# Kernel optimization log

Measured on AMD Instinct MI355X. Metric: run time of the kernel, lower is better.

The kernel has to match this reference:

```python
import jax, jax.numpy as jnp
import numpy as np
from jax import lax

B, C, W, H = 32, 64, 32, 32
HEADS, RED = 4, 16
D = C // HEADS


def setup_inputs() -> dict:
    key = jax.random.key(0)
    ks = jax.random.split(key, 16)
    s = 0.05
    return {
        "x": jax.random.normal(ks[0], (B, C, W, H), jnp.float32),
        "Wq": jax.random.normal(ks[1], (C, C), jnp.float32) * s,
        "bq": jnp.zeros((C,), jnp.float32),
        "Wk": jax.random.normal(ks[2], (C, C), jnp.float32) * s,
        "bk": jnp.zeros((C,), jnp.float32),
        "Wv": jax.random.normal(ks[3], (C, C), jnp.float32) * s,
        "bv": jnp.zeros((C,), jnp.float32),
        "rel_h": jax.random.normal(ks[4], (1, HEADS, D, 1, H), jnp.float32),
        "rel_w": jax.random.normal(ks[5], (1, HEADS, D, W, 1), jnp.float32),
        "ln_g": jnp.ones((C, W, H), jnp.float32),
        "ln_b": jnp.zeros((C, W, H), jnp.float32),
        "ca_w1": jax.random.normal(ks[6], (C // RED, C), jnp.float32) * s,
        "ca_b1": jnp.zeros((C // RED,), jnp.float32),
        "ca_w2": jax.random.normal(ks[7], (C, C // RED), jnp.float32) * s,
        "ca_b2": jnp.zeros((C,), jnp.float32),
        "sa_w": jax.random.normal(ks[8], (1, 2, 7, 7), jnp.float32) * s,
        "sa_b": jnp.zeros((1,), jnp.float32),
    }


def reference(x, Wq, bq, Wk, bk, Wv, bv, rel_h, rel_w, ln_g, ln_b,
              ca_w1, ca_b1, ca_w2, ca_b2, sa_w, sa_b):
    b, c, w, h = x.shape
    n = w * h
    d = c // HEADS

    def conv1x1(t, wt, bt):
        return jnp.einsum('bchw,oc->bohw', t, wt) + bt[None, :, None, None]

    # ---- MHSA branch ----
    q = conv1x1(x, Wq, bq).reshape(b, HEADS, d, n)
    k = conv1x1(x, Wk, bk).reshape(b, HEADS, d, n)
    v = conv1x1(x, Wv, bv).reshape(b, HEADS, d, n)
    cc = jnp.einsum('bhdi,bhdj->bhij', q, k)                  # content-content
    pos = (rel_h + rel_w).reshape(1, HEADS, d, n)              # [1,H,d,N]
    cp = jnp.einsum('zhdi,bhdj->bhij', pos, q)                 # content-position
    att = jax.nn.softmax(cc + cp, axis=-1)                     # [b,H,N,N]
    out = jnp.einsum('bhdj,bhij->bhdi', v, att).reshape(b, c, w, h)
    # LayerNorm over (C,W,H)
    mu = jnp.mean(out, axis=(1, 2, 3), keepdims=True)
    var = jnp.var(out, axis=(1, 2, 3), keepdims=True)
    ln = (out - mu) * lax.rsqrt(var + 1e-5) * ln_g[None] + ln_b[None]
    mhsa = ln + x

    # ---- CBAM branch ----
    avg = jnp.mean(x, axis=(2, 3))                             # [b,c]
    mx = jnp.max(x, axis=(2, 3))

    def mlp(f):
        hid = jax.nn.relu(jnp.einsum('bc,oc->bo', f, ca_w1) + ca_b1)
        return jnp.einsum('bc,oc->bo', hid, ca_w2) + ca_b2

    ch_att = jax.nn.sigmoid(mlp(avg) + mlp(mx))[:, :, None, None]
    xc = ch_att * x
    feat = jnp.stack([jnp.mean(xc, axis=1), jnp.max(xc, axis=1)], axis=1)  # [b,2,w,h]
    sp = lax.conv_general_dilated(feat, sa_w, (1, 1), 'SAME',
                                  dimension_numbers=('NCHW', 'OIHW', 'NCHW'))
    sp = sp + sa_b[None, :, None, None]
    cbam = jax.nn.sigmoid(sp) * xc

    return mhsa + cbam + x
```

## Files before the change

### kernel.cpp

```cpp
#include <hip/hip_runtime.h>

#define BB 32
#define CC 64
#define WW 32
#define HHT 32
#define NH 4
#define DHD 16
#define NN 1024
#define LOG2E 1.4426950408889634f

typedef __attribute__((ext_vector_type(8))) short bf16x8;
typedef __attribute__((ext_vector_type(4))) float f32x4;

__device__ __forceinline__ float wave_sum(float v) {
#pragma unroll
  for (int off = 32; off > 0; off >>= 1) v += __shfl_down(v, off, 64);
  return v;
}
__device__ __forceinline__ float wave_max(float v) {
#pragma unroll
  for (int off = 32; off > 0; off >>= 1) v = fmaxf(v, __shfl_down(v, off, 64));
  return v;
}
__device__ __forceinline__ unsigned bf16pair(float lo, float hi) {
  unsigned a = __float_as_uint(lo), b = __float_as_uint(hi);
  a += 0x7FFFu + ((a >> 16) & 1u);
  b += 0x7FFFu + ((b >> 16) & 1u);
  return (a >> 16) | (b & 0xFFFF0000u);
}
__device__ __forceinline__ unsigned bf16pair_trunc(float lo, float hi) {
  return __builtin_amdgcn_perm(__float_as_uint(hi), __float_as_uint(lo), 0x07060302u);
}
__device__ __forceinline__ short bf16s(float f) {
  unsigned a = __float_as_uint(f);
  a += 0x7FFFu + ((a >> 16) & 1u);
  return (short)(a >> 16);
}

__global__ __launch_bounds__(256) void qkv_kernel(
    const float* __restrict__ x,
    const float* __restrict__ Wq, const float* __restrict__ bq,
    const float* __restrict__ Wk, const float* __restrict__ bk,
    const float* __restrict__ Wv, const float* __restrict__ bv,
    short* __restrict__ KQ, short* __restrict__ Vb, float* __restrict__ lnzero)
{
  __shared__ __align__(16) short Ws[192 * 72];
  const int tid = threadIdx.x;
  const int b = blockIdx.y, nt = blockIdx.x;

  if (tid < 192) {
    const int m = tid >> 4, dd = tid & 15;
    const int mat = m >> 2, h = m & 3;
    const float* src = (mat == 0 ? Wk : (mat == 1 ? Wq : Wv)) + (h * 16 + dd) * CC;
    const float scale = (mat == 0) ? LOG2E : 1.f;
    short* dst = Ws + tid * 72;
#pragma unroll
    for (int c8 = 0; c8 < 8; ++c8) {
      const float4 f0 = *reinterpret_cast<const float4*>(src + c8 * 8);
      const float4 f1 = *reinterpret_cast<const float4*>(src + c8 * 8 + 4);
      uint4 u;
      u.x = bf16pair(f0.x*scale, f0.y*scale); u.y = bf16pair(f0.z*scale, f0.w*scale);
      u.z = bf16pair(f1.x*scale, f1.y*scale); u.w = bf16pair(f1.z*scale, f1.w*scale);
      *reinterpret_cast<uint4*>(dst + c8 * 8) = u;
    }
  }
  if (blockIdx.x == 0 && blockIdx.y == 0 && tid < 64) lnzero[tid] = 0.f;
  __syncthreads();

  const int wid = tid >> 6, lane = tid & 63, Q = lane >> 4, il = lane & 15;
  const int n = nt * 64 + wid * 16 + il;
  const float* xb = x + (size_t)b * CC * NN;

  union { bf16x8 s; unsigned u[4]; } bfr[2];
#pragma unroll
  for (int half = 0; half < 2; ++half) {
#pragma unroll
    for (int p = 0; p < 4; ++p) {
      const int c0 = 32 * half + 8 * Q + 2 * p;
      const float f0 = xb[(size_t)c0 * NN + n];
      const float f1 = xb[(size_t)(c0 + 1) * NN + n];
      bfr[half].u[p] = bf16pair(f0, f1);
    }
  }

  const f32x4 zero4 = {0.f, 0.f, 0.f, 0.f};
  f32x4 acc[12];
#pragma unroll
  for (int m = 0; m < 12; ++m) {
    const short* wr = Ws + (m * 16 + il) * 72;
    const bf16x8 a0 = *reinterpret_cast<const bf16x8*>(wr + 8 * Q);
    const bf16x8 a1 = *reinterpret_cast<const bf16x8*>(wr + 32 + 8 * Q);
    acc[m] = __builtin_amdgcn_mfma_f32_16x16x32_bf16(a0, bfr[0].s, zero4, 0, 0, 0);
    acc[m] = __builtin_amdgcn_mfma_f32_16x16x32_bf16(a1, bfr[1].s, acc[m], 0, 0, 0);
  }

#pragma unroll
  for (int m = 0; m < 12; ++m) {
    const int mat = m >> 2, h = m & 3;
    const float bsc = (mat == 0) ? LOG2E : 1.f;
    const float4 bias = *reinterpret_cast<const float4*>(
        (mat == 0 ? bk : (mat == 1 ? bq : bv)) + h * 16 + 4 * Q);
    const float v0 = acc[m][0] + bias.x*bsc, v1 = acc[m][1] + bias.y*bsc;
    const float v2 = acc[m][2] + bias.z*bsc, v3 = acc[m][3] + bias.w*bsc;
    if (mat < 2) {
      uint2 pk;
      pk.x = bf16pair(v0, v1); pk.y = bf16pair(v2, v3);
      *reinterpret_cast<uint2*>(KQ + ((size_t)(b * NH + h) * NN + n) * 32 +
                                (mat == 0 ? 0 : 16) + 4 * Q) = pk;
    } else {
      short* vb = Vb + ((size_t)(b * NH + h) * 16 + 4 * Q) * NN + n;
      vb[0]            = bf16s(v0);
      vb[(size_t)NN]   = bf16s(v1);
      vb[2*(size_t)NN] = bf16s(v2);
      vb[3*(size_t)NN] = bf16s(v3);
    }
  }
}

__global__ __launch_bounds__(256, 2) void flash_kernel(
    const short* __restrict__ KQ, const short* __restrict__ Vb,
    const float* __restrict__ rel_h, const float* __restrict__ rel_w,
    float* __restrict__ attnout, float* __restrict__ lnsum, float* __restrict__ lnsum2)
{
  const int tid = threadIdx.x;
  const int wid = tid >> 6, lane = tid & 63;
  const int Q = lane >> 4, il = lane & 15;
  const int bh = blockIdx.x;
  const int h = bh & 3, b = bh >> 2;
  const int ibase = blockIdx.y * 256 + wid * 64;

  bf16x8 bfrag[4];
#pragma unroll
  for (int g2 = 0; g2 < 4; ++g2) {
    const int i = ibase + g2*16 + il;
    if (Q < 2) {
      bfrag[g2] = *reinterpret_cast<const bf16x8*>(KQ + ((size_t)bh*NN + i)*32 + 16 + 8*Q);
    } else {
      const int wrow = i >> 5, hcol = i & 31;
      union { bf16x8 s; unsigned u[4]; } t;
#pragma unroll
      for (int p = 0; p < 4; ++p) {
        const int d0 = 8*(Q-2) + 2*p;
        const float f0 = LOG2E*(rel_h[(h*DHD + d0)*HHT + hcol] + rel_w[(h*DHD + d0)*WW + wrow]);
        const float f1 = LOG2E*(rel_h[(h*DHD + d0+1)*HHT + hcol] + rel_w[(h*DHD + d0+1)*WW + wrow]);
        t.u[p] = bf16pair(f0, f1);
      }
      bfrag[g2] = t.s;
    }
  }

  const short* KQb = KQ + (size_t)bh*NN*32;
  const short* Vbb = Vb + ((size_t)bh*16 + il)*NN;
  const f32x4 zero4 = {0.f, 0.f, 0.f, 0.f};
  f32x4 accA[4] = {zero4, zero4, zero4, zero4};
  f32x4 accB[4] = {zero4, zero4, zero4, zero4};
  float lpA[4] = {0.f, 0.f, 0.f, 0.f};
  float lpB[4] = {0.f, 0.f, 0.f, 0.f};

  bf16x8 agA[4], agB[4]; uint2 vloA[2], vhiA[2], vloB[2], vhiB[2];
#pragma unroll
  for (int g = 0; g < 4; ++g) {
    agA[g] = *reinterpret_cast<const bf16x8*>(KQb + (size_t)(      16*g + il)*32 + 8*Q);
    agB[g] = *reinterpret_cast<const bf16x8*>(KQb + (size_t)(512 + 16*g + il)*32 + 8*Q);
  }
#pragma unroll
  for (int hh = 0; hh < 2; ++hh) {
    const short* vpA = Vbb + 32*hh + 4*Q;
    const short* vpB = Vbb + 512 + 32*hh + 4*Q;
    vloA[hh] = *reinterpret_cast<const uint2*>(vpA);
    vhiA[hh] = *reinterpret_cast<const uint2*>(vpA + 16);
    vloB[hh] = *reinterpret_cast<const uint2*>(vpB);
    vhiB[hh] = *reinterpret_cast<const uint2*>(vpB + 16);
  }

  for (int jt = 0; jt < 512; jt += 64) {
    const int jn = (jt + 64) & 511;
    bf16x8 agAn[4], agBn[4]; uint2 vloAn[2], vhiAn[2], vloBn[2], vhiBn[2];
#pragma unroll
    for (int g = 0; g < 4; ++g) {
      agAn[g] = *reinterpret_cast<const bf16x8*>(KQb + (size_t)(      jn + 16*g + il)*32 + 8*Q);
      agBn[g] = *reinterpret_cast<const bf16x8*>(KQb + (size_t)(512 + jn + 16*g + il)*32 + 8*Q);
    }
#pragma unroll
    for (int hh = 0; hh < 2; ++hh) {
      const short* vpA = Vbb + jn + 32*hh + 4*Q;
      const short* vpB = Vbb + 512 + jn + 32*hh + 4*Q;
      vloAn[hh] = *reinterpret_cast<const uint2*>(vpA);
      vhiAn[hh] = *reinterpret_cast<const uint2*>(vpA + 16);
      vloBn[hh] = *reinterpret_cast<const uint2*>(vpB);
      vhiBn[hh] = *reinterpret_cast<const uint2*>(vpB + 16);
    }

    union { bf16x8 s; unsigned u[4]; } bvA0, bvA1, bvB0, bvB1;
    bvA0.u[0] = vloA[0].x; bvA0.u[1] = vloA[0].y; bvA0.u[2] = vhiA[0].x; bvA0.u[3] = vhiA[0].y;
    bvA1.u[0] = vloA[1].x; bvA1.u[1] = vloA[1].y; bvA1.u[2] = vhiA[1].x; bvA1.u[3] = vhiA[1].y;
    bvB0.u[0] = vloB[0].x; bvB0.u[1] = vloB[0].y; bvB0.u[2] = vhiB[0].x; bvB0.u[3] = vhiB[0].y;
    bvB1.u[0] = vloB[1].x; bvB1.u[1] = vloB[1].y; bvB1.u[2] = vhiB[1].x; bvB1.u[3] = vhiB[1].y;

#pragma unroll
    for (int g2 = 0; g2 < 4; ++g2) {
      {
        float p[4][4];
        unsigned pk[4][2];
#pragma unroll
        for (int g = 0; g < 4; ++g) {
          const f32x4 s = __builtin_amdgcn_mfma_f32_16x16x32_bf16(agA[g], bfrag[g2], zero4, 0, 0, 0);
#pragma unroll
          for (int r = 0; r < 4; ++r) p[g][r] = __builtin_amdgcn_exp2f(s[r]);
          lpA[g2] += (p[g][0] + p[g][1]) + (p[g][2] + p[g][3]);
          pk[g][0] = bf16pair_trunc(p[g][0], p[g][1]);
          pk[g][1] = bf16pair_trunc(p[g][2], p[g][3]);
        }
#pragma unroll
        for (int hh = 0; hh < 2; ++hh) {
          union { bf16x8 s; unsigned u[4]; } ap;
          ap.u[0] = pk[2*hh][0];   ap.u[1] = pk[2*hh][1];
          ap.u[2] = pk[2*hh+1][0]; ap.u[3] = pk[2*hh+1][1];
          accA[g2] = __builtin_amdgcn_mfma_f32_16x16x32_bf16(ap.s, hh ? bvA1.s : bvA0.s, accA[g2], 0, 0, 0);
        }
      }
      {
        float p[4][4];
        unsigned pk[4][2];
#pragma unroll
        for (int g = 0; g < 4; ++g) {
          const f32x4 s = __builtin_amdgcn_mfma_f32_16x16x32_bf16(agB[g], bfrag[g2], zero4, 0, 0, 0);
#pragma unroll
          for (int r = 0; r < 4; ++r) p[g][r] = __builtin_amdgcn_exp2f(s[r]);
          lpB[g2] += (p[g][0] + p[g][1]) + (p[g][2] + p[g][3]);
          pk[g][0] = bf16pair_trunc(p[g][0], p[g][1]);
          pk[g][1] = bf16pair_trunc(p[g][2], p[g][3]);
        }
#pragma unroll
        for (int hh = 0; hh < 2; ++hh) {
          union { bf16x8 s; unsigned u[4]; } ap;
          ap.u[0] = pk[2*hh][0];   ap.u[1] = pk[2*hh][1];
          ap.u[2] = pk[2*hh+1][0]; ap.u[3] = pk[2*hh+1][1];
          accB[g2] = __builtin_amdgcn_mfma_f32_16x16x32_bf16(ap.s, hh ? bvB1.s : bvB0.s, accB[g2], 0, 0, 0);
        }
      }
    }
#pragma unroll
    for (int g = 0; g < 4; ++g) { agA[g] = agAn[g]; agB[g] = agBn[g]; }
#pragma unroll
    for (int hh = 0; hh < 2; ++hh) {
      vloA[hh] = vloAn[hh]; vhiA[hh] = vhiAn[hh];
      vloB[hh] = vloBn[hh]; vhiB[hh] = vhiBn[hh];
    }
  }

  float s1 = 0.f, s2 = 0.f;
#pragma unroll
  for (int g2 = 0; g2 < 4; ++g2) {
    float l = lpA[g2] + lpB[g2];
    l += __shfl_xor(l, 16, 64);
    l += __shfl_xor(l, 32, 64);
#pragma unroll
    for (int r = 0; r < 4; ++r) {
      const float li = __shfl(l, 4*Q + r, 64);
      const float v = (accA[g2][r] + accB[g2][r]) / li;
      const int ig = ibase + g2*16 + 4*Q + r;
      attnout[((size_t)b*CC + h*DHD + il)*NN + ig] = v;
      s1 += v; s2 += v*v;
    }
  }
  s1 = wave_sum(s1); s2 = wave_sum(s2);
  __shared__ float r1[4], r2[4];
  if (lane == 0) { r1[wid] = s1; r2[wid] = s2; }
  __syncthreads();
  if (tid == 0) {
    atomicAdd(&lnsum[b],  r1[0]+r1[1]+r1[2]+r1[3]);
    atomicAdd(&lnsum2[b], r2[0]+r2[1]+r2[2]+r2[3]);
  }
}

__global__ __launch_bounds__(256) void cbamstats_kernel(
    const float* __restrict__ x, float* __restrict__ avg, float* __restrict__ mx)
{
  const int bc = blockIdx.x, tid = threadIdx.x;
  const float* p = x + (size_t)bc*NN;
  float s = 0.f, m = -3.0e38f;
  for (int u = tid; u < NN; u += 256) { const float v = p[u]; s += v; m = fmaxf(m, v); }
  s = wave_sum(s); m = wave_max(m);
  __shared__ float rs[4], rm[4];
  const int wid = tid >> 6, lane = tid & 63;
  if (lane == 0) { rs[wid] = s; rm[wid] = m; }
  __syncthreads();
  if (tid == 0) {
    avg[bc] = (rs[0]+rs[1]+rs[2]+rs[3]) * (1.f/NN);
    mx[bc]  = fmaxf(fmaxf(rm[0], rm[1]), fmaxf(rm[2], rm[3]));
  }
}

__global__ __launch_bounds__(256) void mlpfeat_kernel(
    const float* __restrict__ x, const float* __restrict__ avg, const float* __restrict__ mxv,
    const float* __restrict__ w1, const float* __restrict__ b1,
    const float* __restrict__ w2, const float* __restrict__ b2,
    float* __restrict__ chv, float* __restrict__ feat)
{
  const int b = blockIdx.y, qq = blockIdx.x, tid = threadIdx.x;
  __shared__ float sa[CC], sm[CC], sch[CC];
  __shared__ float ps[4][64], pm[4][64];
  if (tid < CC) { sa[tid] = avg[b*CC + tid]; sm[tid] = mxv[b*CC + tid]; }
  __syncthreads();
  if (tid < CC) {
    float s = 2.f * b2[tid];
#pragma unroll
    for (int o = 0; o < 4; ++o) {
      float ha = b1[o], hm = b1[o];
#pragma unroll
      for (int k = 0; k < CC; ++k) { ha += w1[o*CC + k]*sa[k]; hm += w1[o*CC + k]*sm[k]; }
      s += w2[tid*4 + o] * (fmaxf(ha, 0.f) + fmaxf(hm, 0.f));
    }
    const float c = 1.f/(1.f + __expf(-s));
    sch[tid] = c;
    if (qq == 0) chv[b*CC + tid] = c;
  }
  __syncthreads();
  const int nl = tid & 63, cg = tid >> 6;
  const int n = qq*64 + nl;
  float s = 0.f, m = -3.0e38f;
#pragma unroll
  for (int c = cg*16; c < cg*16 + 16; ++c) {
    const float v = sch[c] * x[((size_t)b*CC + c)*NN + n];
    s += v; m = fmaxf(m, v);
  }
  ps[cg][nl] = s; pm[cg][nl] = m;
  __syncthreads();
  if (cg == 0) {
    const float S = ps[0][nl]+ps[1][nl]+ps[2][nl]+ps[3][nl];
    const float M = fmaxf(fmaxf(pm[0][nl], pm[1][nl]), fmaxf(pm[2][nl], pm[3][nl]));
    feat[(size_t)b*2*NN + n]      = S * (1.f/CC);
    feat[(size_t)b*2*NN + NN + n] = M;
  }
}

__global__ __launch_bounds__(256) void final_kernel(
    const float* __restrict__ x, const float* __restrict__ attn,
    const float* __restrict__ ln_g, const float* __restrict__ ln_b,
    const float* __restrict__ feat, const float* __restrict__ ch,
    const float* __restrict__ lnsum, const float* __restrict__ lnsum2,
    const float* __restrict__ sa_w, const float* __restrict__ sa_b,
    float* __restrict__ out)
{
  const int b = blockIdx.y;
  const int c0 = blockIdx.z * 8;
  const int n = blockIdx.x*256 + threadIdx.x;
  const int w = n >> 5, hh = n & 31;
  __shared__ float sch[CC];
  __shared__ float swt[98];
  if (threadIdx.x < CC) sch[threadIdx.x] = ch[b*CC + threadIdx.x];
  if (threadIdx.x < 98) swt[threadIdx.x] = sa_w[threadIdx.x];
  __syncthreads();

  float s = sa_b[0];
#pragma unroll
  for (int ci = 0; ci < 2; ++ci)
#pragma unroll
    for (int kh = 0; kh < 7; ++kh) {
      const int wy = w + kh - 3;
      if (wy < 0 || wy >= WW) continue;
#pragma unroll
      for (int kw = 0; kw < 7; ++kw) {
        const int hx = hh + kw - 3;
        if (hx < 0 || hx >= HHT) continue;
        s += feat[((size_t)(b*2) + ci)*NN + wy*HHT + hx] * swt[ci*49 + kh*7 + kw];
      }
    }
  const float sg = 1.f/(1.f + __expf(-s));
  const float inv = 1.f/(CC*NN);
  const float m = lnsum[b]*inv;
  const float var = lnsum2[b]*inv - m*m;
  const float r = rsqrtf(var + 1e-5f);
#pragma unroll
  for (int c = c0; c < c0 + 8; ++c) {
    const size_t idx = ((size_t)b*CC + c)*NN + n;
    const float xa = x[idx];
    const float ln = (attn[idx] - m) * r * ln_g[c*NN + n] + ln_b[c*NN + n];
    out[idx] = ln + 2.f*xa + sg * sch[c] * xa;
  }
}

extern "C" void kernel_launch(void* const* d_in, const int* in_sizes, int n_in,
                              void* d_out, int out_size, void* d_ws, size_t ws_size,
                              hipStream_t stream)
{
  const float* x     = (const float*)d_in[0];
  const float* Wq    = (const float*)d_in[1];
  const float* bq    = (const float*)d_in[2];
  const float* Wk    = (const float*)d_in[3];
  const float* bk    = (const float*)d_in[4];
  const float* Wv    = (const float*)d_in[5];
  const float* bv    = (const float*)d_in[6];
  const float* rel_h = (const float*)d_in[7];
  const float* rel_w = (const float*)d_in[8];
  const float* ln_g  = (const float*)d_in[9];
  const float* ln_b  = (const float*)d_in[10];
  const float* cw1   = (const float*)d_in[11];
  const float* cb1   = (const float*)d_in[12];
  const float* cw2   = (const float*)d_in[13];
  const float* cb2   = (const float*)d_in[14];
  const float* saw   = (const float*)d_in[15];
  const float* sab   = (const float*)d_in[16];
  float* out = (float*)d_out;

  short* KQ = (short*)d_ws;
  short* Vb = KQ + (size_t)128*1024*32;
  float* fs = (float*)(Vb + (size_t)128*16*1024);
  float* lnsum  = fs;
  float* lnsum2 = fs + 32;
  float* avg    = fs + 64;
  float* mxv    = avg + 2048;
  float* chv    = mxv + 2048;
  float* feat   = chv + 2048;
  float* attn   = out;

  qkv_kernel<<<dim3(16, BB), 256, 0, stream>>>(x, Wq, bq, Wk, bk, Wv, bv, KQ, Vb, lnsum);
  flash_kernel<<<dim3(BB*NH, 4), 256, 0, stream>>>(KQ, Vb, rel_h, rel_w, attn, lnsum, lnsum2);
  cbamstats_kernel<<<BB*CC, 256, 0, stream>>>(x, avg, mxv);
  mlpfeat_kernel<<<dim3(16, BB), 256, 0, stream>>>(x, avg, mxv, cw1, cb1, cw2, cb2, chv, feat);
  final_kernel<<<dim3(4, BB, 8), 256, 0, stream>>>(x, attn, ln_g, ln_b, feat, chv, lnsum, lnsum2, saw, sab, out);
}
```

Before: 175.2 us.

## Split key range across two wave groups and merge partial attention through LDS

The flash kernel now launches 512 threads per block. The two halves of the block each process half of the key/value range for the same 256 queries, which doubles the number of waves in flight to hide exp and MFMA latency. Partial outputs and row sums are combined in shared memory, then written with coalesced float4 stores using a reciprocal instead of a divide. The cost is extra LDS traffic, a block barrier, and higher register pressure from the tighter launch bounds.

```diff
diff --git a/kernel.cpp b/kernel.cpp
--- a/kernel.cpp
+++ b/kernel.cpp
@@ -11,6 +11,8 @@
 
 typedef __attribute__((ext_vector_type(8))) short bf16x8;
 typedef __attribute__((ext_vector_type(4))) float f32x4;
+
+union vfrag_t { bf16x8 s; uint2 d[2]; unsigned u[4]; };
 
 __device__ __forceinline__ float wave_sum(float v) {
 #pragma unroll
@@ -117,17 +119,24 @@
   }
 }
 
-__global__ __launch_bounds__(256, 2) void flash_kernel(
+#define OSTRIDE 260
+__global__ __launch_bounds__(512, 4) void flash_kernel(
     const short* __restrict__ KQ, const short* __restrict__ Vb,
     const float* __restrict__ rel_h, const float* __restrict__ rel_w,
     float* __restrict__ attnout, float* __restrict__ lnsum, float* __restrict__ lnsum2)
 {
+  __shared__ __align__(16) float Olds[2*16*OSTRIDE];
+  __shared__ float lpl[2*256];
+  __shared__ float r1[8], r2[8];
   const int tid = threadIdx.x;
   const int wid = tid >> 6, lane = tid & 63;
   const int Q = lane >> 4, il = lane & 15;
+  const int jh = wid >> 2, iquad = wid & 3;
   const int bh = blockIdx.x;
   const int h = bh & 3, b = bh >> 2;
-  const int ibase = blockIdx.y * 256 + wid * 64;
+  const int iblk = blockIdx.y * 256;
+  const int ibase = iblk + iquad * 64;
+  const int jbase = jh * 512;
 
   bf16x8 bfrag[4];
 #pragma unroll
@@ -137,7 +146,7 @@
       bfrag[g2] = *reinterpret_cast<const bf16x8*>(KQ + ((size_t)bh*NN + i)*32 + 16 + 8*Q);
     } else {
       const int wrow = i >> 5, hcol = i & 31;
-      union { bf16x8 s; unsigned u[4]; } t;
+      vfrag_t t;
 #pragma unroll
       for (int p = 0; p < 4; ++p) {
         const int d0 = 8*(Q-2) + 2*p;
@@ -149,53 +158,49 @@
     }
   }
 
-  const short* KQb = KQ + (size_t)bh*NN*32;
-  const short* Vbb = Vb + ((size_t)bh*16 + il)*NN;
+  const short* KQb = KQ + (size_t)bh*NN*32 + (size_t)jbase*32;
+  const short* Vbb = Vb + ((size_t)bh*16 + il)*NN + jbase;
   const f32x4 zero4 = {0.f, 0.f, 0.f, 0.f};
   f32x4 accA[4] = {zero4, zero4, zero4, zero4};
   f32x4 accB[4] = {zero4, zero4, zero4, zero4};
   float lpA[4] = {0.f, 0.f, 0.f, 0.f};
   float lpB[4] = {0.f, 0.f, 0.f, 0.f};
 
-  bf16x8 agA[4], agB[4]; uint2 vloA[2], vhiA[2], vloB[2], vhiB[2];
+  bf16x8 agA[4], agB[4];
+  vfrag_t bvA[2], bvB[2];
 #pragma unroll
   for (int g = 0; g < 4; ++g) {
     agA[g] = *reinterpret_cast<const bf16x8*>(KQb + (size_t)(      16*g + il)*32 + 8*Q);
-    agB[g] = *reinterpret_cast<const bf16x8*>(KQb + (size_t)(512 + 16*g + il)*32 + 8*Q);
+    agB[g] = *reinterpret_cast<const bf16x8*>(KQb + (size_t)(256 + 16*g + il)*32 + 8*Q);
   }
 #pragma unroll
   for (int hh = 0; hh < 2; ++hh) {
     const short* vpA = Vbb + 32*hh + 4*Q;
-    const short* vpB = Vbb + 512 + 32*hh + 4*Q;
-    vloA[hh] = *reinterpret_cast<const uint2*>(vpA);
-    vhiA[hh] = *reinterpret_cast<const uint2*>(vpA + 16);
-    vloB[hh] = *reinterpret_cast<const uint2*>(vpB);
-    vhiB[hh] = *reinterpret_cast<const uint2*>(vpB + 16);
-  }
-
-  for (int jt = 0; jt < 512; jt += 64) {
-    const int jn = (jt + 64) & 511;
-    bf16x8 agAn[4], agBn[4]; uint2 vloAn[2], vhiAn[2], vloBn[2], vhiBn[2];
+    const short* vpB = Vbb + 256 + 32*hh + 4*Q;
+    bvA[hh].d[0] = *reinterpret_cast<const uint2*>(vpA);
+    bvA[hh].d[1] = *reinterpret_cast<const uint2*>(vpA + 16);
+    bvB[hh].d[0] = *reinterpret_cast<const uint2*>(vpB);
+    bvB[hh].d[1] = *reinterpret_cast<const uint2*>(vpB + 16);
+  }
+
+  for (int jt = 0; jt < 256; jt += 64) {
+    const int jn = (jt + 64) & 255;
+    bf16x8 agAn[4], agBn[4];
+    vfrag_t bvAn[2], bvBn[2];
 #pragma unroll
     for (int g = 0; g < 4; ++g) {
       agAn[g] = *reinterpret_cast<const bf16x8*>(KQb + (size_t)(      jn + 16*g + il)*32 + 8*Q);
-      agBn[g] = *reinterpret_cast<const bf16x8*>(KQb + (size_t)(512 + jn + 16*g + il)*32 + 8*Q);
+      agBn[g] = *reinterpret_cast<const bf16x8*>(KQb + (size_t)(256 + jn + 16*g + il)*32 + 8*Q);
     }
 #pragma unroll
     for (int hh = 0; hh < 2; ++hh) {
       const short* vpA = Vbb + jn + 32*hh + 4*Q;
-      const short* vpB = Vbb + 512 + jn + 32*hh + 4*Q;
-      vloAn[hh] = *reinterpret_cast<const uint2*>(vpA);
-      vhiAn[hh] = *reinterpret_cast<const uint2*>(vpA + 16);
-      vloBn[hh] = *reinterpret_cast<const uint2*>(vpB);
-      vhiBn[hh] = *reinterpret_cast<const uint2*>(vpB + 16);
-    }
-
-    union { bf16x8 s; unsigned u[4]; } bvA0, bvA1, bvB0, bvB1;
-    bvA0.u[0] = vloA[0].x; bvA0.u[1] = vloA[0].y; bvA0.u[2] = vhiA[0].x; bvA0.u[3] = vhiA[0].y;
-    bvA1.u[0] = vloA[1].x; bvA1.u[1] = vloA[1].y; bvA1.u[2] = vhiA[1].x; bvA1.u[3] = vhiA[1].y;
-    bvB0.u[0] = vloB[0].x; bvB0.u[1] = vloB[0].y; bvB0.u[2] = vhiB[0].x; bvB0.u[3] = vhiB[0].y;
-    bvB1.u[0] = vloB[1].x; bvB1.u[1] = vloB[1].y; bvB1.u[2] = vhiB[1].x; bvB1.u[3] = vhiB[1].y;
+      const short* vpB = Vbb + 256 + jn + 32*hh + 4*Q;
+      bvAn[hh].d[0] = *reinterpret_cast<const uint2*>(vpA);
+      bvAn[hh].d[1] = *reinterpret_cast<const uint2*>(vpA + 16);
+      bvBn[hh].d[0] = *reinterpret_cast<const uint2*>(vpB);
+      bvBn[hh].d[1] = *reinterpret_cast<const uint2*>(vpB + 16);
+    }
 
 #pragma unroll
     for (int g2 = 0; g2 < 4; ++g2) {
@@ -213,10 +218,10 @@
         }
 #pragma unroll
         for (int hh = 0; hh < 2; ++hh) {
-          union { bf16x8 s; unsigned u[4]; } ap;
+          vfrag_t ap;
           ap.u[0] = pk[2*hh][0];   ap.u[1] = pk[2*hh][1];
           ap.u[2] = pk[2*hh+1][0]; ap.u[3] = pk[2*hh+1][1];
-          accA[g2] = __builtin_amdgcn_mfma_f32_16x16x32_bf16(ap.s, hh ? bvA1.s : bvA0.s, accA[g2], 0, 0, 0);
+          accA[g2] = __builtin_amdgcn_mfma_f32_16x16x32_bf16(ap.s, bvA[hh].s, accA[g2], 0, 0, 0);
         }
       }
       {
@@ -233,44 +238,56 @@
         }
 #pragma unroll
         for (int hh = 0; hh < 2; ++hh) {
-          union { bf16x8 s; unsigned u[4]; } ap;
+          vfrag_t ap;
           ap.u[0] = pk[2*hh][0];   ap.u[1] = pk[2*hh][1];
           ap.u[2] = pk[2*hh+1][0]; ap.u[3] = pk[2*hh+1][1];
-          accB[g2] = __builtin_amdgcn_mfma_f32_16x16x32_bf16(ap.s, hh ? bvB1.s : bvB0.s, accB[g2], 0, 0, 0);
+          accB[g2] = __builtin_amdgcn_mfma_f32_16x16x32_bf16(ap.s, bvB[hh].s, accB[g2], 0, 0, 0);
         }
       }
     }
 #pragma unroll
     for (int g = 0; g < 4; ++g) { agA[g] = agAn[g]; agB[g] = agBn[g]; }
 #pragma unroll
-    for (int hh = 0; hh < 2; ++hh) {
-      vloA[hh] = vloAn[hh]; vhiA[hh] = vhiAn[hh];
-      vloB[hh] = vloBn[hh]; vhiB[hh] = vhiBn[hh];
-    }
-  }
-
-  float s1 = 0.f, s2 = 0.f;
+    for (int hh = 0; hh < 2; ++hh) { bvA[hh] = bvAn[hh]; bvB[hh] = bvBn[hh]; }
+  }
+
 #pragma unroll
   for (int g2 = 0; g2 < 4; ++g2) {
     float l = lpA[g2] + lpB[g2];
     l += __shfl_xor(l, 16, 64);
     l += __shfl_xor(l, 32, 64);
-#pragma unroll
-    for (int r = 0; r < 4; ++r) {
-      const float li = __shfl(l, 4*Q + r, 64);
-      const float v = (accA[g2][r] + accB[g2][r]) / li;
-      const int ig = ibase + g2*16 + 4*Q + r;
-      attnout[((size_t)b*CC + h*DHD + il)*NN + ig] = v;
-      s1 += v; s2 += v*v;
-    }
+    if (Q == 0) lpl[jh*256 + iquad*64 + g2*16 + il] = l;
+    float* od = Olds + (jh*16 + il)*OSTRIDE + iquad*64 + g2*16 + 4*Q;
+#pragma unroll
+    for (int r = 0; r < 4; ++r) od[r] = accA[g2][r] + accB[g2][r];
+  }
+  __syncthreads();
+
+  float s1 = 0.f, s2 = 0.f;
+#pragma unroll
+  for (int pass = 0; pass < 2; ++pass) {
+    const int d = (tid >> 6) + 8*pass;
+    const int i0 = (tid & 63)*4;
+    const float4 a = *reinterpret_cast<const float4*>(&Olds[(0*16 + d)*OSTRIDE + i0]);
+    const float4 c = *reinterpret_cast<const float4*>(&Olds[(1*16 + d)*OSTRIDE + i0]);
+    float4 v;
+    v.x = (a.x + c.x) * __builtin_amdgcn_rcpf(lpl[i0+0] + lpl[256+i0+0]);
+    v.y = (a.y + c.y) * __builtin_amdgcn_rcpf(lpl[i0+1] + lpl[256+i0+1]);
+    v.z = (a.z + c.z) * __builtin_amdgcn_rcpf(lpl[i0+2] + lpl[256+i0+2]);
+    v.w = (a.w + c.w) * __builtin_amdgcn_rcpf(lpl[i0+3] + lpl[256+i0+3]);
+    *reinterpret_cast<float4*>(&attnout[((size_t)b*CC + h*DHD + d)*NN + iblk + i0]) = v;
+    s1 += (v.x + v.y) + (v.z + v.w);
+    s2 += (v.x*v.x + v.y*v.y) + (v.z*v.z + v.w*v.w);
   }
   s1 = wave_sum(s1); s2 = wave_sum(s2);
-  __shared__ float r1[4], r2[4];
   if (lane == 0) { r1[wid] = s1; r2[wid] = s2; }
   __syncthreads();
   if (tid == 0) {
-    atomicAdd(&lnsum[b],  r1[0]+r1[1]+r1[2]+r1[3]);
-    atomicAdd(&lnsum2[b], r2[0]+r2[1]+r2[2]+r2[3]);
+    float a1 = 0.f, a2 = 0.f;
+#pragma unroll
+    for (int w = 0; w < 8; ++w) { a1 += r1[w]; a2 += r2[w]; }
+    atomicAdd(&lnsum[b], a1);
+    atomicAdd(&lnsum2[b], a2);
   }
 }
 
@@ -416,7 +433,7 @@
   float* attn   = out;
 
   qkv_kernel<<<dim3(16, BB), 256, 0, stream>>>(x, Wq, bq, Wk, bk, Wv, bv, KQ, Vb, lnsum);
-  flash_kernel<<<dim3(BB*NH, 4), 256, 0, stream>>>(KQ, Vb, rel_h, rel_w, attn, lnsum, lnsum2);
+  flash_kernel<<<dim3(BB*NH, 4), 512, 0, stream>>>(KQ, Vb, rel_h, rel_w, attn, lnsum, lnsum2);
   cbamstats_kernel<<<BB*CC, 256, 0, stream>>>(x, avg, mxv);
   mlpfeat_kernel<<<dim3(16, BB), 256, 0, stream>>>(x, avg, mxv, cw1, cb1, cw2, cb2, chv, feat);
   final_kernel<<<dim3(4, BB, 8), 256, 0, stream>>>(x, attn, ln_g, ln_b, feat, chv, lnsum, lnsum2, saw, sab, out);
```

Result: slower. 273.2 us (+55.9%).
